# Kernel optimization log

Hardware: AMD Instinct MI355X
Metric: run time of the kernel (lower is better)

The kernel has to match this reference:

```python
import jax, jax.numpy as jnp
import numpy as np

B, L, D = 64, 1024, 64  # (batch*heads, seq_len, head_dim)


def setup_inputs() -> dict:
    key = jax.random.key(0)
    kq, kk, kv = jax.random.split(key, 3)
    q = jax.random.normal(kq, (B, L, D), dtype=jnp.float32)
    k = jax.random.normal(kk, (B, L, D), dtype=jnp.float32)
    v = jax.random.normal(kv, (B, L, D), dtype=jnp.float32)
    scale = jnp.float32(1.0 / np.sqrt(D))  # standard 1/sqrt(d_head)
    return {"q": q, "k": k, "v": v, "scale": scale}


def reference(q, k, v, scale):
    # attention = bmm(q, k^T) * scale  -> [B, L, L]
    attention = jnp.einsum("bqd,bkd->bqk", q, k) * scale
    # softmax over dim=2 (keys); dropout p=0.0 is identity
    attention = jax.nn.softmax(attention, axis=2)
    # context = bmm(attention, v) -> [B, L, D]
    context = jnp.einsum("bqk,bkd->bqd", attention, v)
    return (context, attention)
```

## Files before the change

kernel.cpp:

```cpp
#include <hip/hip_runtime.h>
#include <hip/hip_bf16.h>

typedef __bf16 bf16x8 __attribute__((ext_vector_type(8)));
typedef __bf16 bf16x4 __attribute__((ext_vector_type(4)));
typedef float  f32x4  __attribute__((ext_vector_type(4)));

#define NB 64
#define LL 1024
#define DD 64
#define PB 40

#define NW 16
#define LDS_K_BYTES (LL * DD * 2)
#define LDS_TOTAL   (LDS_K_BYTES + NW * 16 * PB * 2)

#if __has_builtin(__builtin_amdgcn_exp2f)
#define EXP2(x) __builtin_amdgcn_exp2f(x)
#else
#define EXP2(x) exp2f(x)
#endif

__global__ __launch_bounds__(256)
void preconvert_v(const float* __restrict__ v, __bf16* __restrict__ vt) {
  const int blk = blockIdx.x, tid = threadIdx.x;
  const int b = blk >> 4, t = blk & 15;
  __shared__ float tile[64][65];
  const float* src = v + ((size_t)b * LL + t * 64) * DD;
  for (int i = tid; i < 64 * 16; i += 256) {
    const int row = i >> 4, c4 = (i & 15) * 4;
    f32x4 x = *(const f32x4*)(src + row * DD + c4);
    tile[row][c4 + 0] = x[0]; tile[row][c4 + 1] = x[1];
    tile[row][c4 + 2] = x[2]; tile[row][c4 + 3] = x[3];
  }
  __syncthreads();
  __bf16* dst = vt + (size_t)b * DD * LL + t * 64;
  for (int i = tid; i < 64 * 8; i += 256) {
    const int d = i >> 3, k8 = (i & 7) * 8;
    bf16x8 o;
    #pragma unroll
    for (int j = 0; j < 8; ++j) o[j] = (__bf16)tile[k8 + j][d];
    *(bf16x8*)(dst + (size_t)d * LL + k8) = o;
  }
}

__global__ __launch_bounds__(1024, 1)
void sdpa_wide(const float* __restrict__ q, const float* __restrict__ kf,
               const __bf16* __restrict__ vt, const float* __restrict__ scale_p,
               float* __restrict__ out) {
  extern __shared__ char smem[];
  __bf16* Klds = (__bf16*)smem;
  __bf16* Pw   = (__bf16*)(smem + LDS_K_BYTES);

  const int tid  = threadIdx.x;
  const int lane = tid & 63;
  const int w    = tid >> 6;
  const int l15  = lane & 15;
  const int lg   = lane >> 4;

  int bid = blockIdx.x;
  bid = (bid & 7) * 32 + (bid >> 3);
  const int b     = bid >> 2;
  const int qrow0 = (bid & 3) * 256 + w * 16;

  const float scale2 = scale_p[0] * 1.4426950408889634f;
  const float* kb = kf + (size_t)b * LL * DD;
  const __bf16* vb = vt + (size_t)b * DD * LL;
  float* ctxb  = out + ((size_t)b * LL + qrow0) * DD;
  float* attnb = out + (size_t)NB * LL * DD + (size_t)b * LL * LL
               + (size_t)qrow0 * LL;

  #pragma unroll
  for (int it = 0; it < 8; ++it) {
    const int c = it * 1024 + tid;
    const int row = c >> 3, slot = c & 7;
    const f32x4* s4 = (const f32x4*)(kb + (size_t)c * 8);
    f32x4 x0 = s4[0], x1 = s4[1];
    bf16x8 t;
    #pragma unroll
    for (int j = 0; j < 4; ++j) { t[j] = (__bf16)x0[j]; t[4 + j] = (__bf16)x1[j]; }
    *(bf16x8*)(Klds + row * 64 + ((slot * 8) ^ ((row & 7) * 8))) = t;
  }

  bf16x8 aq[2];
  {
    const float* qrow = q + ((size_t)b * LL + qrow0 + l15) * DD;
    #pragma unroll
    for (int s = 0; s < 2; ++s) {
      const f32x4* p4 = (const f32x4*)(qrow + s * 32 + lg * 8);
      f32x4 x0 = p4[0], x1 = p4[1];
      #pragma unroll
      for (int j = 0; j < 4; ++j) {
        aq[s][j]     = (__bf16)(x0[j] * scale2);
        aq[s][4 + j] = (__bf16)(x1[j] * scale2);
      }
    }
  }

  __syncthreads();

  const int xsw  = (l15 & 7) * 8;
  const int woff = (w * 2) & 31;
  __bf16* prow = Pw + (w * 16 + l15) * PB;

  float ls = 0.f;
  for (int kt = 0; kt < 32; ++kt) {
    const int kk = (kt + woff) & 31;
    bf16x8 bk[2][2];
    #pragma unroll
    for (int f = 0; f < 2; ++f)
      #pragma unroll
      for (int s = 0; s < 2; ++s)
        bk[f][s] = *(const bf16x8*)(Klds + (kk * 32 + f * 16 + l15) * 64
                                         + ((s * 32 + lg * 8) ^ xsw));
    f32x4 sacc[2] = {{0.f,0.f,0.f,0.f},{0.f,0.f,0.f,0.f}};
    #pragma unroll
    for (int s = 0; s < 2; ++s)
      #pragma unroll
      for (int f = 0; f < 2; ++f)
        sacc[f] = __builtin_amdgcn_mfma_f32_16x16x32_bf16(bk[f][s], aq[s], sacc[f], 0, 0, 0);
    #pragma unroll
    for (int f = 0; f < 2; ++f)
      #pragma unroll
      for (int r = 0; r < 4; ++r)
        ls += EXP2(sacc[f][r]);
  }
  ls += __shfl_xor(ls, 16, 64);
  ls += __shfl_xor(ls, 32, 64);
  const float rl = 1.0f / ls;

  f32x4 cacc[4];
  #pragma unroll
  for (int g = 0; g < 4; ++g) cacc[g] = (f32x4){0.f, 0.f, 0.f, 0.f};

  bf16x8 bvA[4], bvB[4];
  {
    const int k0 = woff, k1 = (woff + 1) & 31;
    #pragma unroll
    for (int g = 0; g < 4; ++g) {
      bvA[g] = *(const bf16x8*)(vb + (size_t)(g * 16 + l15) * LL + k0 * 32 + lg * 8);
      bvB[g] = *(const bf16x8*)(vb + (size_t)(g * 16 + l15) * LL + k1 * 32 + lg * 8);
    }
  }

  for (int kt = 0; kt < 32; ++kt) {
    const int kk  = (kt + woff) & 31;
    const int kk2 = (kt + 2 + woff) & 31;

    bf16x8 bvc[4];
    #pragma unroll
    for (int g = 0; g < 4; ++g) bvc[g] = bvA[g];
    #pragma unroll
    for (int g = 0; g < 4; ++g) bvA[g] = bvB[g];
    #pragma unroll
    for (int g = 0; g < 4; ++g)
      bvB[g] = *(const bf16x8*)(vb + (size_t)(g * 16 + l15) * LL + kk2 * 32 + lg * 8);

    bf16x8 bk[2][2];
    #pragma unroll
    for (int f = 0; f < 2; ++f)
      #pragma unroll
      for (int s = 0; s < 2; ++s)
        bk[f][s] = *(const bf16x8*)(Klds + (kk * 32 + f * 16 + l15) * 64
                                         + ((s * 32 + lg * 8) ^ xsw));

    f32x4 sacc[2] = {{0.f,0.f,0.f,0.f},{0.f,0.f,0.f,0.f}};
    #pragma unroll
    for (int s = 0; s < 2; ++s)
      #pragma unroll
      for (int f = 0; f < 2; ++f)
        sacc[f] = __builtin_amdgcn_mfma_f32_16x16x32_bf16(bk[f][s], aq[s], sacc[f], 0, 0, 0);

    f32x4 pv[2];
    #pragma unroll
    for (int f = 0; f < 2; ++f)
      #pragma unroll
      for (int r = 0; r < 4; ++r)
        pv[f][r] = EXP2(sacc[f][r]) * rl;

    #pragma unroll
    for (int f = 0; f < 2; ++f) {
      bf16x4 pb;
      #pragma unroll
      for (int r = 0; r < 4; ++r) pb[r] = (__bf16)pv[f][r];
      *(bf16x4*)(prow + f * 16 + lg * 4) = pb;
    }
    bf16x8 pa = *(const bf16x8*)(prow + lg * 8);
    #pragma unroll
    for (int g = 0; g < 4; ++g)
      cacc[g] = __builtin_amdgcn_mfma_f32_16x16x32_bf16(pa, bvc[g], cacc[g], 0, 0, 0);

    float* arow = attnb + (size_t)l15 * LL + kk * 32 + lg * 4;
    __builtin_nontemporal_store(pv[0], (f32x4*)arow);
    __builtin_nontemporal_store(pv[1], (f32x4*)(arow + 16));
  }

  #pragma unroll
  for (int g = 0; g < 4; ++g)
    #pragma unroll
    for (int r = 0; r < 4; ++r)
      ctxb[(size_t)(lg * 4 + r) * DD + g * 16 + l15] = cacc[g][r];
}

#define BQ 64
#define BK 32
#define KSTRIDE 72
#define VSTRIDE 40
#define PSTRIDE 48

__global__ __launch_bounds__(256, 4)
void sdpa_fallback(const float* __restrict__ q, const float* __restrict__ k,
                   const float* __restrict__ v, const float* __restrict__ scale_p,
                   float* __restrict__ out) {
  const int tid  = threadIdx.x;
  const int lane = tid & 63;
  const int w    = tid >> 6;
  int bid = blockIdx.x;
  bid = (bid & 7) * 128 + (bid >> 3);
  const int b    = bid >> 4;
  const int qblk = (bid & 15) * BQ;

  __shared__ __bf16 Ks[BK * KSTRIDE];
  __shared__ __bf16 Vs[DD * VSTRIDE];
  __shared__ __bf16 Pp[4][16 * PSTRIDE];

  const float scale = scale_p[0];
  const float* qb = q + ((size_t)b * LL + qblk) * DD;
  const float* kb = k + (size_t)b * LL * DD;
  const float* vb = v + (size_t)b * LL * DD;
  float* ctx  = out + ((size_t)b * LL + qblk) * DD;
  float* attn = out + (size_t)NB * LL * DD + (size_t)b * LL * LL + (size_t)qblk * LL;

  const int l15 = lane & 15;
  const int lg  = lane >> 4;
  const int dchunk = lg * 8;

  bf16x8 aq[2];
  {
    const float* qrow = qb + (size_t)(w * 16 + l15) * DD;
    #pragma unroll
    for (int s = 0; s < 2; ++s) {
      const f32x4* p4 = (const f32x4*)(qrow + s * 32 + dchunk);
      f32x4 x0 = p4[0], x1 = p4[1];
      #pragma unroll
      for (int j = 0; j < 4; ++j) {
        aq[s][j]     = (__bf16)(x0[j] * scale);
        aq[s][4 + j] = (__bf16)(x1[j] * scale);
      }
    }
  }

  const int srow = tid >> 3;
  const int sd0  = (tid & 7) * 8;

  float lpart[4] = {0.f, 0.f, 0.f, 0.f};
  for (int kt = 0; kt < LL / BK; ++kt) {
    __syncthreads();
    {
      const f32x4* src = (const f32x4*)(kb + (size_t)(kt * BK + srow) * DD + sd0);
      f32x4 x0 = src[0], x1 = src[1];
      bf16x8 t;
      #pragma unroll
      for (int j = 0; j < 4; ++j) { t[j] = (__bf16)x0[j]; t[4 + j] = (__bf16)x1[j]; }
      *(bf16x8*)&Ks[srow * KSTRIDE + sd0] = t;
    }
    __syncthreads();
    f32x4 sacc[2] = {{0.f,0.f,0.f,0.f},{0.f,0.f,0.f,0.f}};
    #pragma unroll
    for (int s = 0; s < 2; ++s)
      #pragma unroll
      for (int f = 0; f < 2; ++f) {
        bf16x8 bk = *(const bf16x8*)&Ks[(f * 16 + l15) * KSTRIDE + s * 32 + dchunk];
        sacc[f] = __builtin_amdgcn_mfma_f32_16x16x32_bf16(aq[s], bk, sacc[f], 0, 0, 0);
      }
    #pragma unroll
    for (int f = 0; f < 2; ++f)
      #pragma unroll
      for (int r = 0; r < 4; ++r)
        lpart[r] += __expf(sacc[f][r]);
  }
  #pragma unroll
  for (int m = 1; m < 16; m <<= 1)
    #pragma unroll
    for (int r = 0; r < 4; ++r)
      lpart[r] += __shfl_xor(lpart[r], m, 64);
  float rl[4];
  #pragma unroll
  for (int r = 0; r < 4; ++r) rl[r] = 1.0f / lpart[r];

  f32x4 cacc[4] = {{0.f,0.f,0.f,0.f},{0.f,0.f,0.f,0.f},
                   {0.f,0.f,0.f,0.f},{0.f,0.f,0.f,0.f}};
  for (int kt = 0; kt < LL / BK; ++kt) {
    __syncthreads();
    {
      const f32x4* src = (const f32x4*)(kb + (size_t)(kt * BK + srow) * DD + sd0);
      f32x4 x0 = src[0], x1 = src[1];
      bf16x8 t;
      #pragma unroll
      for (int j = 0; j < 4; ++j) { t[j] = (__bf16)x0[j]; t[4 + j] = (__bf16)x1[j]; }
      *(bf16x8*)&Ks[srow * KSTRIDE + sd0] = t;
      const f32x4* vsrc = (const f32x4*)(vb + (size_t)(kt * BK + srow) * DD + sd0);
      f32x4 y0 = vsrc[0], y1 = vsrc[1];
      #pragma unroll
      for (int j = 0; j < 4; ++j) {
        Vs[(sd0 + j)     * VSTRIDE + srow] = (__bf16)y0[j];
        Vs[(sd0 + 4 + j) * VSTRIDE + srow] = (__bf16)y1[j];
      }
    }
    __syncthreads();
    f32x4 sacc[2] = {{0.f,0.f,0.f,0.f},{0.f,0.f,0.f,0.f}};
    #pragma unroll
    for (int s = 0; s < 2; ++s)
      #pragma unroll
      for (int f = 0; f < 2; ++f) {
        bf16x8 bk = *(const bf16x8*)&Ks[(f * 16 + l15) * KSTRIDE + s * 32 + dchunk];
        sacc[f] = __builtin_amdgcn_mfma_f32_16x16x32_bf16(aq[s], bk, sacc[f], 0, 0, 0);
      }
    #pragma unroll
    for (int f = 0; f < 2; ++f)
      #pragma unroll
      for (int r = 0; r < 4; ++r) {
        const int row = lg * 4 + r;
        float p = __expf(sacc[f][r]) * rl[r];
        attn[(size_t)(w * 16 + row) * LL + (kt * BK + f * 16 + l15)] = p;
        Pp[w][row * PSTRIDE + f * 16 + l15] = (__bf16)p;
      }
    bf16x8 pa = *(const bf16x8*)&Pp[w][l15 * PSTRIDE + lg * 8];
    #pragma unroll
    for (int g = 0; g < 4; ++g) {
      bf16x8 bv = *(const bf16x8*)&Vs[(g * 16 + l15) * VSTRIDE + lg * 8];
      cacc[g] = __builtin_amdgcn_mfma_f32_16x16x32_bf16(pa, bv, cacc[g], 0, 0, 0);
    }
  }
  #pragma unroll
  for (int g = 0; g < 4; ++g)
    #pragma unroll
    for (int r = 0; r < 4; ++r)
      ctx[(size_t)(w * 16 + lg * 4 + r) * DD + g * 16 + l15] = cacc[g][r];
}

extern "C" void kernel_launch(void* const* d_in, const int* in_sizes, int n_in,
                              void* d_out, int out_size, void* d_ws, size_t ws_size,
                              hipStream_t stream) {
  const float* q = (const float*)d_in[0];
  const float* k = (const float*)d_in[1];
  const float* v = (const float*)d_in[2];
  const float* s = (const float*)d_in[3];
  float* out = (float*)d_out;

  const size_t vbytes = (size_t)NB * LL * DD * 2;
  if (ws_size >= vbytes) {
    __bf16* vt = (__bf16*)d_ws;
    preconvert_v<<<dim3(NB * (LL / 64)), dim3(256), 0, stream>>>(v, vt);
    (void)hipFuncSetAttribute((const void*)sdpa_wide,
                              hipFuncAttributeMaxDynamicSharedMemorySize,
                              LDS_TOTAL);
    sdpa_wide<<<dim3(256), dim3(1024), LDS_TOTAL, stream>>>(q, k, vt, s, out);
  } else {
    sdpa_fallback<<<dim3(NB * (LL / 64)), dim3(256), 0, stream>>>(q, k, v, s, out);
  }
}
```

Baseline: 123.2 us.

## Split attention into 256-thread blocks with streamed bf16 K tiles

Replaces the 1024-thread, one-block-per-CU kernel that staged all of K in LDS with 256-thread blocks (up to four per CU) that each own 64 query rows and stream K through LDS in 256-row chunks. K is now converted to bf16 once in a combined preconvert kernel with V, so the main kernel reads bf16 K instead of converting fp32 K per block. The aim is better occupancy and latency hiding across more, smaller blocks. The cost is reloading K for both passes in every block, extra barriers, dropping the V register double-buffering and rotated tile order, and using plain instead of nontemporal stores for the attention matrix.

```diff
diff --git a/kernel.cpp b/kernel.cpp
--- a/kernel.cpp
+++ b/kernel.cpp
@@ -10,9 +10,9 @@
 #define DD 64
 #define PB 40
 
-#define NW 16
-#define LDS_K_BYTES (LL * DD * 2)
-#define LDS_TOTAL   (LDS_K_BYTES + NW * 16 * PB * 2)
+#define WS_VT_OFF 0
+#define WS_KB_OFF ((size_t)8 * 1024 * 1024)
+#define WS_NEED   ((size_t)16 * 1024 * 1024)
 
 #if __has_builtin(__builtin_amdgcn_exp2f)
 #define EXP2(x) __builtin_amdgcn_exp2f(x)
@@ -21,35 +21,45 @@
 #endif
 
 __global__ __launch_bounds__(256)
-void preconvert_v(const float* __restrict__ v, __bf16* __restrict__ vt) {
+void preconvert_kv(const float* __restrict__ k, const float* __restrict__ v,
+                   __bf16* __restrict__ kbf, __bf16* __restrict__ vt) {
   const int blk = blockIdx.x, tid = threadIdx.x;
-  const int b = blk >> 4, t = blk & 15;
-  __shared__ float tile[64][65];
-  const float* src = v + ((size_t)b * LL + t * 64) * DD;
-  for (int i = tid; i < 64 * 16; i += 256) {
-    const int row = i >> 4, c4 = (i & 15) * 4;
-    f32x4 x = *(const f32x4*)(src + row * DD + c4);
-    tile[row][c4 + 0] = x[0]; tile[row][c4 + 1] = x[1];
-    tile[row][c4 + 2] = x[2]; tile[row][c4 + 3] = x[3];
-  }
-  __syncthreads();
-  __bf16* dst = vt + (size_t)b * DD * LL + t * 64;
-  for (int i = tid; i < 64 * 8; i += 256) {
-    const int d = i >> 3, k8 = (i & 7) * 8;
+  if (blk < NB * (LL / 64)) {
+    const int b = blk >> 4, t = blk & 15;
+    __shared__ float tile[64][65];
+    const float* src = v + ((size_t)b * LL + t * 64) * DD;
+    for (int i = tid; i < 64 * 16; i += 256) {
+      const int row = i >> 4, c4 = (i & 15) * 4;
+      f32x4 x = *(const f32x4*)(src + row * DD + c4);
+      tile[row][c4 + 0] = x[0]; tile[row][c4 + 1] = x[1];
+      tile[row][c4 + 2] = x[2]; tile[row][c4 + 3] = x[3];
+    }
+    __syncthreads();
+    __bf16* dst = vt + (size_t)b * DD * LL + t * 64;
+    for (int i = tid; i < 64 * 8; i += 256) {
+      const int d = i >> 3, k8 = (i & 7) * 8;
+      bf16x8 o;
+      #pragma unroll
+      for (int j = 0; j < 8; ++j) o[j] = (__bf16)tile[k8 + j][d];
+      *(bf16x8*)(dst + (size_t)d * LL + k8) = o;
+    }
+  } else {
+    const size_t base = ((size_t)(blk - 1024) * 256 + tid) * 8;
+    const f32x4* s = (const f32x4*)(k + base);
+    f32x4 x0 = s[0], x1 = s[1];
     bf16x8 o;
     #pragma unroll
-    for (int j = 0; j < 8; ++j) o[j] = (__bf16)tile[k8 + j][d];
-    *(bf16x8*)(dst + (size_t)d * LL + k8) = o;
+    for (int j = 0; j < 4; ++j) { o[j] = (__bf16)x0[j]; o[4 + j] = (__bf16)x1[j]; }
+    *(bf16x8*)(kbf + base) = o;
   }
 }
 
-__global__ __launch_bounds__(1024, 1)
-void sdpa_wide(const float* __restrict__ q, const float* __restrict__ kf,
-               const __bf16* __restrict__ vt, const float* __restrict__ scale_p,
-               float* __restrict__ out) {
-  extern __shared__ char smem[];
-  __bf16* Klds = (__bf16*)smem;
-  __bf16* Pw   = (__bf16*)(smem + LDS_K_BYTES);
+__global__ __launch_bounds__(256, 4)
+void sdpa_quarter(const float* __restrict__ q, const __bf16* __restrict__ kbf,
+                  const __bf16* __restrict__ vt, const float* __restrict__ scale_p,
+                  float* __restrict__ out) {
+  __shared__ __bf16 Kq[256 * 64];
+  __shared__ __bf16 Pw[4 * 16 * PB];
 
   const int tid  = threadIdx.x;
   const int lane = tid & 63;
@@ -58,29 +68,17 @@
   const int lg   = lane >> 4;
 
   int bid = blockIdx.x;
-  bid = (bid & 7) * 32 + (bid >> 3);
-  const int b     = bid >> 2;
-  const int qrow0 = (bid & 3) * 256 + w * 16;
+  bid = (bid & 7) * 128 + (bid >> 3);
+  const int b     = bid >> 4;
+  const int qrow0 = (bid & 15) * 64 + w * 16;
 
   const float scale2 = scale_p[0] * 1.4426950408889634f;
-  const float* kb = kf + (size_t)b * LL * DD;
-  const __bf16* vb = vt + (size_t)b * DD * LL;
+  const __bf16* kb = kbf + (size_t)b * LL * DD;
+  const __bf16* vb = vt  + (size_t)b * DD * LL;
   float* ctxb  = out + ((size_t)b * LL + qrow0) * DD;
   float* attnb = out + (size_t)NB * LL * DD + (size_t)b * LL * LL
                + (size_t)qrow0 * LL;
 
-  #pragma unroll
-  for (int it = 0; it < 8; ++it) {
-    const int c = it * 1024 + tid;
-    const int row = c >> 3, slot = c & 7;
-    const f32x4* s4 = (const f32x4*)(kb + (size_t)c * 8);
-    f32x4 x0 = s4[0], x1 = s4[1];
-    bf16x8 t;
-    #pragma unroll
-    for (int j = 0; j < 4; ++j) { t[j] = (__bf16)x0[j]; t[4 + j] = (__bf16)x1[j]; }
-    *(bf16x8*)(Klds + row * 64 + ((slot * 8) ^ ((row & 7) * 8))) = t;
-  }
-
   bf16x8 aq[2];
   {
     const float* qrow = q + ((size_t)b * LL + qrow0 + l15) * DD;
@@ -96,33 +94,40 @@
     }
   }
 
-  __syncthreads();
-
-  const int xsw  = (l15 & 7) * 8;
-  const int woff = (w * 2) & 31;
+  const int xsw = (l15 & 7) * 8;
   __bf16* prow = Pw + (w * 16 + l15) * PB;
 
   float ls = 0.f;
-  for (int kt = 0; kt < 32; ++kt) {
-    const int kk = (kt + woff) & 31;
-    bf16x8 bk[2][2];
-    #pragma unroll
-    for (int f = 0; f < 2; ++f)
+  for (int qt = 0; qt < 4; ++qt) {
+    __syncthreads();
+    #pragma unroll
+    for (int it = 0; it < 8; ++it) {
+      const int c = it * 256 + tid;
+      const int row = c >> 3, slot = c & 7;
+      bf16x8 t = *(const bf16x8*)(kb + (size_t)(qt * 256 + row) * 64 + slot * 8);
+      *(bf16x8*)(Kq + row * 64 + ((slot * 8) ^ ((row & 7) * 8))) = t;
+    }
+    __syncthreads();
+    for (int kt = 0; kt < 8; ++kt) {
+      bf16x8 bk[2][2];
+      #pragma unroll
+      for (int f = 0; f < 2; ++f)
+        #pragma unroll
+        for (int s = 0; s < 2; ++s)
+          bk[f][s] = *(const bf16x8*)(Kq + (kt * 32 + f * 16 + l15) * 64
+                                         + ((s * 32 + lg * 8) ^ xsw));
+      f32x4 sacc[2] = {{0.f,0.f,0.f,0.f},{0.f,0.f,0.f,0.f}};
       #pragma unroll
       for (int s = 0; s < 2; ++s)
-        bk[f][s] = *(const bf16x8*)(Klds + (kk * 32 + f * 16 + l15) * 64
-                                         + ((s * 32 + lg * 8) ^ xsw));
-    f32x4 sacc[2] = {{0.f,0.f,0.f,0.f},{0.f,0.f,0.f,0.f}};
-    #pragma unroll
-    for (int s = 0; s < 2; ++s)
+        #pragma unroll
+        for (int f = 0; f < 2; ++f)
+          sacc[f] = __builtin_amdgcn_mfma_f32_16x16x32_bf16(bk[f][s], aq[s], sacc[f], 0, 0, 0);
       #pragma unroll
       for (int f = 0; f < 2; ++f)
-        sacc[f] = __builtin_amdgcn_mfma_f32_16x16x32_bf16(bk[f][s], aq[s], sacc[f], 0, 0, 0);
-    #pragma unroll
-    for (int f = 0; f < 2; ++f)
-      #pragma unroll
-      for (int r = 0; r < 4; ++r)
-        ls += EXP2(sacc[f][r]);
+        #pragma unroll
+        for (int r = 0; r < 4; ++r)
+          ls += EXP2(sacc[f][r]);
+    }
   }
   ls += __shfl_xor(ls, 16, 64);
   ls += __shfl_xor(ls, 32, 64);
@@ -132,66 +137,62 @@
   #pragma unroll
   for (int g = 0; g < 4; ++g) cacc[g] = (f32x4){0.f, 0.f, 0.f, 0.f};
 
-  bf16x8 bvA[4], bvB[4];
-  {
-    const int k0 = woff, k1 = (woff + 1) & 31;
-    #pragma unroll
-    for (int g = 0; g < 4; ++g) {
-      bvA[g] = *(const bf16x8*)(vb + (size_t)(g * 16 + l15) * LL + k0 * 32 + lg * 8);
-      bvB[g] = *(const bf16x8*)(vb + (size_t)(g * 16 + l15) * LL + k1 * 32 + lg * 8);
-    }
-  }
-
-  for (int kt = 0; kt < 32; ++kt) {
-    const int kk  = (kt + woff) & 31;
-    const int kk2 = (kt + 2 + woff) & 31;
-
-    bf16x8 bvc[4];
-    #pragma unroll
-    for (int g = 0; g < 4; ++g) bvc[g] = bvA[g];
-    #pragma unroll
-    for (int g = 0; g < 4; ++g) bvA[g] = bvB[g];
-    #pragma unroll
-    for (int g = 0; g < 4; ++g)
-      bvB[g] = *(const bf16x8*)(vb + (size_t)(g * 16 + l15) * LL + kk2 * 32 + lg * 8);
-
-    bf16x8 bk[2][2];
-    #pragma unroll
-    for (int f = 0; f < 2; ++f)
+  for (int qt = 0; qt < 4; ++qt) {
+    __syncthreads();
+    #pragma unroll
+    for (int it = 0; it < 8; ++it) {
+      const int c = it * 256 + tid;
+      const int row = c >> 3, slot = c & 7;
+      bf16x8 t = *(const bf16x8*)(kb + (size_t)(qt * 256 + row) * 64 + slot * 8);
+      *(bf16x8*)(Kq + row * 64 + ((slot * 8) ^ ((row & 7) * 8))) = t;
+    }
+    __syncthreads();
+
+    for (int kt = 0; kt < 8; ++kt) {
+      bf16x8 bv[4];
+      #pragma unroll
+      for (int g = 0; g < 4; ++g)
+        bv[g] = *(const bf16x8*)(vb + (size_t)(g * 16 + l15) * LL
+                                    + qt * 256 + kt * 32 + lg * 8);
+
+      bf16x8 bk[2][2];
+      #pragma unroll
+      for (int f = 0; f < 2; ++f)
+        #pragma unroll
+        for (int s = 0; s < 2; ++s)
+          bk[f][s] = *(const bf16x8*)(Kq + (kt * 32 + f * 16 + l15) * 64
+                                         + ((s * 32 + lg * 8) ^ xsw));
+
+      f32x4 sacc[2] = {{0.f,0.f,0.f,0.f},{0.f,0.f,0.f,0.f}};
       #pragma unroll
       for (int s = 0; s < 2; ++s)
-        bk[f][s] = *(const bf16x8*)(Klds + (kk * 32 + f * 16 + l15) * 64
-                                         + ((s * 32 + lg * 8) ^ xsw));
-
-    f32x4 sacc[2] = {{0.f,0.f,0.f,0.f},{0.f,0.f,0.f,0.f}};
-    #pragma unroll
-    for (int s = 0; s < 2; ++s)
+        #pragma unroll
+        for (int f = 0; f < 2; ++f)
+          sacc[f] = __builtin_amdgcn_mfma_f32_16x16x32_bf16(bk[f][s], aq[s], sacc[f], 0, 0, 0);
+
+      f32x4 pv[2];
       #pragma unroll
       for (int f = 0; f < 2; ++f)
-        sacc[f] = __builtin_amdgcn_mfma_f32_16x16x32_bf16(bk[f][s], aq[s], sacc[f], 0, 0, 0);
-
-    f32x4 pv[2];
-    #pragma unroll
-    for (int f = 0; f < 2; ++f)
-      #pragma unroll
-      for (int r = 0; r < 4; ++r)
-        pv[f][r] = EXP2(sacc[f][r]) * rl;
-
-    #pragma unroll
-    for (int f = 0; f < 2; ++f) {
-      bf16x4 pb;
-      #pragma unroll
-      for (int r = 0; r < 4; ++r) pb[r] = (__bf16)pv[f][r];
-      *(bf16x4*)(prow + f * 16 + lg * 4) = pb;
-    }
-    bf16x8 pa = *(const bf16x8*)(prow + lg * 8);
-    #pragma unroll
-    for (int g = 0; g < 4; ++g)
-      cacc[g] = __builtin_amdgcn_mfma_f32_16x16x32_bf16(pa, bvc[g], cacc[g], 0, 0, 0);
-
-    float* arow = attnb + (size_t)l15 * LL + kk * 32 + lg * 4;
-    __builtin_nontemporal_store(pv[0], (f32x4*)arow);
-    __builtin_nontemporal_store(pv[1], (f32x4*)(arow + 16));
+        #pragma unroll
+        for (int r = 0; r < 4; ++r)
+          pv[f][r] = EXP2(sacc[f][r]) * rl;
+
+      float* arow = attnb + (size_t)l15 * LL + qt * 256 + kt * 32 + lg * 4;
+      *(f32x4*)(arow)      = pv[0];
+      *(f32x4*)(arow + 16) = pv[1];
+
+      #pragma unroll
+      for (int f = 0; f < 2; ++f) {
+        bf16x4 pb;
+        #pragma unroll
+        for (int r = 0; r < 4; ++r) pb[r] = (__bf16)pv[f][r];
+        *(bf16x4*)(prow + f * 16 + lg * 4) = pb;
+      }
+      bf16x8 pa = *(const bf16x8*)(prow + lg * 8);
+      #pragma unroll
+      for (int g = 0; g < 4; ++g)
+        cacc[g] = __builtin_amdgcn_mfma_f32_16x16x32_bf16(pa, bv[g], cacc[g], 0, 0, 0);
+    }
   }
 
   #pragma unroll
@@ -347,14 +348,11 @@
   const float* s = (const float*)d_in[3];
   float* out = (float*)d_out;
 
-  const size_t vbytes = (size_t)NB * LL * DD * 2;
-  if (ws_size >= vbytes) {
-    __bf16* vt = (__bf16*)d_ws;
-    preconvert_v<<<dim3(NB * (LL / 64)), dim3(256), 0, stream>>>(v, vt);
-    (void)hipFuncSetAttribute((const void*)sdpa_wide,
-                              hipFuncAttributeMaxDynamicSharedMemorySize,
-                              LDS_TOTAL);
-    sdpa_wide<<<dim3(256), dim3(1024), LDS_TOTAL, stream>>>(q, k, vt, s, out);
+  if (ws_size >= WS_NEED) {
+    __bf16* vt  = (__bf16*)((char*)d_ws + WS_VT_OFF);
+    __bf16* kbf = (__bf16*)((char*)d_ws + WS_KB_OFF);
+    preconvert_kv<<<dim3(3072), dim3(256), 0, stream>>>(k, v, kbf, vt);
+    sdpa_quarter<<<dim3(1024), dim3(256), 0, stream>>>(q, kbf, vt, s, out);
   } else {
     sdpa_fallback<<<dim3(NB * (LL / 64)), dim3(256), 0, stream>>>(q, k, v, s, out);
   }
```

Measured after the change: 113.0 us. 8.3% less time.
